# Performance work log

Hardware: AMD Instinct MI355X
Metric: run time of the kernel (lower is better)

## Reference

```python
import jax, jax.numpy as jnp
import numpy as np

N_QUBITS = 12
LAYERS = 3


def _apply(state, mats, axes):
    """Apply batched k-qubit gate. state: [B]+[2]*n complex64; mats: [B, 2^k, 2^k]; axes: state axes (1-based)."""
    k = len(axes)
    d = 2 ** k
    s = jnp.moveaxis(state, axes, tuple(range(1, k + 1)))
    shp = s.shape
    s = jnp.einsum('bij,bjk->bik', mats, s.reshape(shp[0], d, -1))
    return jnp.moveaxis(s.reshape(shp), tuple(range(1, k + 1)), axes)


def _ry(theta):
    # RY(theta) = [[cos(t/2), -sin(t/2)], [sin(t/2), cos(t/2)]], batched over B
    c = jnp.cos(theta / 2).astype(jnp.complex64)
    s = jnp.sin(theta / 2).astype(jnp.complex64)
    return jnp.stack([jnp.stack([c, -s], -1), jnp.stack([s, c], -1)], -2)


def _crx(theta):
    # CRX: identity on control=0 subspace, RX(theta) on control=1 subspace (basis order |ct>)
    c = jnp.cos(theta / 2).astype(jnp.complex64)
    s = (-1j) * jnp.sin(theta / 2).astype(jnp.complex64)
    o = jnp.ones_like(c)
    z = jnp.zeros_like(c)
    rows = [[o, z, z, z], [z, o, z, z], [z, z, c, s], [z, z, s, c]]
    return jnp.stack([jnp.stack(r, -1) for r in rows], -2)


def _circuit(state_re, state_im, params):
    B = params.shape[0]
    n = N_QUBITS
    state = (state_re + 1j * state_im).astype(jnp.complex64).reshape((B,) + (2,) * n)
    p = params.reshape(B, LAYERS, 4, n)  # param idx order: RY block, CRX block, RY block, CRX block
    for l in range(LAYERS):
        th = p[:, l]
        for w in range(n):
            state = _apply(state, _ry(th[:, 0, w]), (w + 1,))
        for i, w in enumerate(reversed(range(n))):
            state = _apply(state, _crx(th[:, 1, i]), (w + 1, ((w + 1) % n) + 1))
        for w in range(n):
            state = _apply(state, _ry(th[:, 2, w]), (w + 1,))
        for i, w in enumerate([n - 1] + list(range(n - 1))):
            state = _apply(state, _crx(th[:, 3, i]), (w + 1, ((w - 1) % n) + 1))
    state = state.reshape(B, -1)
    return jnp.stack([state.real, state.imag], -1)  # [B, 2^n, 2]


def setup_inputs() -> dict:
    key = jax.random.key(0)
    k1, k2, k3 = jax.random.split(key, 3)
    B = 128
    dim = 2 ** N_QUBITS
    return {
        'state_re': jax.random.normal(k1, (B, dim), jnp.float32),
        'state_im': jax.random.normal(k2, (B, dim), jnp.float32),
        'params': jax.random.normal(k3, (B, LAYERS * 4 * N_QUBITS), jnp.float32),
    }


def reference(state_re, state_im, params):
    return _circuit(state_re, state_im, params)
```

## Files before the change

### kernel.cpp

```cpp
#include <hip/hip_runtime.h>
#include <math.h>

#define DIM  4096
#define BLK  512
#define NPAR 144

typedef float v2f __attribute__((ext_vector_type(2)));

struct Ph { int reg[3]; int wav[3]; };
struct TMap { unsigned pk[9]; unsigned short so[8]; unsigned short rn[8]; };

constexpr int REGS[12][3] = {
  {11,0,1},{1,2,3},{3,4,5},{5,6,7},{7,8,9},{9,10,11},
  {11,0,1},{9,10,11},{7,8,9},{5,6,7},{3,4,5},{1,2,3}};

constexpr Ph phaseAt(int i) {
  Ph p = {};
  if (i == 0 || i == 37) {
    p.reg[0]=0; p.reg[1]=1; p.reg[2]=2;
    p.wav[0]=9; p.wav[1]=10; p.wav[2]=11;
    return p;
  }
  int e = (i - 1) % 12;
  for (int j = 0; j < 3; ++j) p.reg[j] = REGS[e][j];
  bool A = (e <= 2) || (e >= 10);
  p.wav[0] = A ? 6 : 2; p.wav[1] = A ? 7 : 3; p.wav[2] = A ? 8 : 4;
  return p;
}
constexpr bool inArr(const int* a, int n, int b) {
  for (int i = 0; i < n; ++i) if (a[i] == b) return true;
  return false;
}
constexpr int idxOf3(const int* a, int v) {
  for (int j = 0; j < 3; ++j) if (a[j] == v) return j;
  return -1;
}
constexpr bool isLoc(int t) {
  if (t == 0 || t == 36) return false;
  Ph a = phaseAt(t), b = phaseAt(t + 1);
  return a.wav[0]==b.wav[0] && a.wav[1]==b.wav[1] && a.wav[2]==b.wav[2];
}
constexpr int bufIdx(int t) {
  int k = 0;
  for (int u = 0; u <= t; ++u) if (!isLoc(u)) ++k;
  return (k + 1) & 1;
}
constexpr int sharedBit(Ph o, Ph n) {
  for (int j = 0; j < 3; ++j) if (inArr(n.reg, 3, o.reg[j])) return o.reg[j];
  return -1;
}

struct BuildOut { TMap m; int js, jn; bool ok; };

constexpr BuildOut buildT(Ph o, Ph n, bool local) {
  BuildOut R = {};
  R.ok = true;
  int s = sharedBit(o, n);
  if (s < 0) { R.ok = false; return R; }
  R.js = idxOf3(o.reg, s);
  R.jn = idxOf3(n.reg, s);
  if (R.js < 0 || R.jn < 0) { R.ok = false; return R; }
  bool lo[12] = {}, ln[12] = {};
  for (int b = 0; b < 12; ++b) {
    lo[b] = !inArr(o.reg,3,b) && !inArr(o.wav,3,b);
    ln[b] = !inArr(n.reg,3,b) && !inArr(n.wav,3,b);
  }
  int col[12] = {};
  bool uo[12] = {}, un[12] = {}, consumed[12] = {};
  col[s] = 1; consumed[s] = true;
  int row = 1;
  for (int b = 0; b < 12 && row < 4; ++b)
    if (lo[b] && ln[b] && !consumed[b]) { col[b] = 1 << row; uo[b]=un[b]=true; consumed[b]=true; ++row; }
  while (row < 4) {
    int a = -1, c = -1;
    for (int b = 0; b < 12; ++b) if (lo[b] && !uo[b] && !consumed[b]) { a = b; break; }
    for (int b = 0; b < 12; ++b) if (ln[b] && !un[b] && !consumed[b] && b != a) { c = b; break; }
    if (a < 0 || c < 0) { R.ok = false; return R; }
    col[a] |= 1 << row; col[c] |= 1 << row;
    uo[a]=true; un[c]=true; consumed[c]=true;
    ++row;
  }
  if (local) {
    for (int i = 0; i < 3; ++i) {
      if (consumed[o.wav[i]]) { R.ok = false; return R; }
      col[o.wav[i]] |= 1 << (9 + i);
      consumed[o.wav[i]] = true;
    }
    int rr = 4;
    for (int b = 0; b < 12; ++b) if (!consumed[b]) { col[b] |= 1 << rr; ++rr; }
    if (rr != 9) { R.ok = false; return R; }
  } else {
    int rr = 4;
    for (int b = 0; b < 12; ++b) if (!consumed[b]) { col[b] |= 1 << rr; ++rr; }
    if (rr != 12) { R.ok = false; return R; }
  }
  {
    int pv[12] = {}, pb[12] = {};
    int nr = 0;
    for (int b = 0; b < 12; ++b) {
      int v = col[b];
      for (int k = 0; k < nr; ++k) if (v & pb[k]) v ^= pv[k];
      if (v) { pb[nr] = v & (-v); pv[nr] = v; ++nr; }
    }
    if (nr != 12) { R.ok = false; return R; }
  }
  int Lo[6] = {}, Ln[6] = {};
  int i0 = 0, i1 = 0;
  for (int b = 0; b < 12; ++b) { if (lo[b]) Lo[i0++] = b; if (ln[b]) Ln[i1++] = b; }
  if (i0 != 6 || i1 != 6) { R.ok = false; return R; }
  for (int i = 0; i < 9; ++i) {
    unsigned po = (i < 6) ? (unsigned)col[Lo[i]] : (unsigned)col[o.wav[i-6]];
    unsigned pn = (i < 6) ? (unsigned)col[Ln[i]] : (unsigned)col[n.wav[i-6]];
    R.m.pk[i] = po | (pn << 16);
  }
  for (int r = 0; r < 8; ++r) {
    int a = 0, c = 0;
    for (int j = 0; j < 3; ++j)
      if ((r >> j) & 1) { a ^= col[o.reg[j]]; c ^= col[n.reg[j]]; }
    R.m.so[r] = (unsigned short)(a * 8);
    R.m.rn[r] = (unsigned short)(c * 8);
  }
  return R;
}

struct AllT { TMap t[37]; bool loc[37]; int buf[37]; int js[37]; int jn[37]; bool ok; };
constexpr AllT buildAll() {
  AllT A = {};
  A.ok = true;
  for (int t = 0; t < 37; ++t) {
    BuildOut b = buildT(phaseAt(t), phaseAt(t + 1), isLoc(t));
    A.t[t] = b.m;
    A.ok = A.ok && b.ok;
    A.loc[t] = isLoc(t);
    A.buf[t] = bufIdx(t);
    A.js[t] = b.js;
    A.jn[t] = b.jn;
  }
  return A;
}
constexpr AllT AT = buildAll();
static_assert(AT.ok, "slot-map construction failed");

__device__ __forceinline__ float rlf(float v, int l) {
  return __int_as_float(__builtin_amdgcn_readlane(__float_as_int(v), l));
}
template<int AO>
__device__ __forceinline__ v2f angAt(const float (&ct)[3], const float (&st)[3]) {
  v2f a;
  a.x = rlf(ct[AO >> 6], AO & 63);
  a.y = rlf(st[AO >> 6], AO & 63);
  return a;
}

template<int J>
__device__ __forceinline__ void ry8(v2f (&z)[8], v2f a) {
  const float c = a.x, s = a.y;
  #pragma unroll
  for (int p = 0; p < 4; ++p) {
    const int r0 = ((p & ~((1 << J) - 1)) << 1) | (p & ((1 << J) - 1));
    const int r1 = r0 | (1 << J);
    v2f u = z[r0], v = z[r1];
    z[r0] = c * u - s * v;
    z[r1] = s * u + c * v;
  }
}
template<int JC, int JT>
__device__ __forceinline__ void crx8(v2f (&z)[8], v2f a) {
  const float c = a.x, s = a.y;
  constexpr int MC = 1 << JC, MT = 1 << JT;
  constexpr int mlo = MC < MT ? MC : MT;
  constexpr int mhi = MC < MT ? MT : MC;
  #pragma unroll
  for (int p = 0; p < 2; ++p) {
    int q = ((p & ~(mlo - 1)) << 1) | (p & (mlo - 1));
    q = ((q & ~(mhi - 1)) << 1) | (q & (mhi - 1));
    const int r0 = q | MC, r1 = r0 | MT;
    v2f u = z[r0], v = z[r1];
    v2f n0, n1;
    n0.x = c * u.x + s * v.y;
    n0.y = c * u.y - s * v.x;
    n1.x = c * v.x + s * u.y;
    n1.y = c * v.y - s * u.x;
    z[r0] = n0; z[r1] = n1;
  }
}

template<int E, int L>
__device__ __forceinline__ void gates(v2f (&z)[8], const float (&ct)[3], const float (&st)[3]) {
#define A(k) (angAt<48 * L + (k)>(ct, st))
  if constexpr (E == 0)      { ry8<0>(z,A(0));  ry8<1>(z,A(11)); ry8<2>(z,A(10));
                               crx8<1,0>(z,A(12)); crx8<2,1>(z,A(13)); }
  else if constexpr (E == 1) { ry8<1>(z,A(9));  ry8<2>(z,A(8));
                               crx8<1,0>(z,A(14)); crx8<2,1>(z,A(15)); }
  else if constexpr (E == 2) { ry8<1>(z,A(7));  ry8<2>(z,A(6));
                               crx8<1,0>(z,A(16)); crx8<2,1>(z,A(17)); }
  else if constexpr (E == 3) { ry8<1>(z,A(5));  ry8<2>(z,A(4));
                               crx8<1,0>(z,A(18)); crx8<2,1>(z,A(19)); }
  else if constexpr (E == 4) { ry8<1>(z,A(3));  ry8<2>(z,A(2));
                               crx8<1,0>(z,A(20)); crx8<2,1>(z,A(21)); }
  else if constexpr (E == 5) { ry8<1>(z,A(1));
                               crx8<1,0>(z,A(22)); crx8<2,1>(z,A(23)); }
  else if constexpr (E == 6) { ry8<0>(z,A(24)); ry8<1>(z,A(35)); ry8<2>(z,A(34));
                               crx8<1,2>(z,A(36)); crx8<0,1>(z,A(37)); }
  else if constexpr (E == 7) { ry8<0>(z,A(26)); ry8<1>(z,A(25));
                               crx8<1,2>(z,A(38)); crx8<0,1>(z,A(39)); }
  else if constexpr (E == 8) { ry8<0>(z,A(28)); ry8<1>(z,A(27));
                               crx8<1,2>(z,A(40)); crx8<0,1>(z,A(41)); }
  else if constexpr (E == 9) { ry8<0>(z,A(30)); ry8<1>(z,A(29));
                               crx8<1,2>(z,A(42)); crx8<0,1>(z,A(43)); }
  else if constexpr (E == 10){ ry8<0>(z,A(32)); ry8<1>(z,A(31));
                               crx8<1,2>(z,A(44)); crx8<0,1>(z,A(45)); }
  else                       { ry8<1>(z,A(33));
                               crx8<1,2>(z,A(46)); crx8<0,1>(z,A(47)); }
#undef A
}

template<int T>
__device__ __forceinline__ void restage(v2f (&z)[8], int tid, char* Lb, char* C0, char* C1) {
  constexpr bool LOC = AT.loc[T];
  constexpr int JS = AT.js[T], JN = AT.jn[T];
  char* buf = LOC ? Lb : (AT.buf[T] ? C1 : C0);
  unsigned acc = 0;
  #pragma unroll
  for (int i = 0; i < 9; ++i)
    acc ^= (unsigned)(-((tid >> i) & 1)) & AT.t[T].pk[i];
  const unsigned bo = (acc & 0xfffu) << 3;
  const unsigned bn = ((acc >> 16) & 0xfffu) << 3;
  #pragma unroll
  for (int r = 0; r < 8; ++r) {
    if (r & (1 << JS)) continue;
    v2f z0 = z[r], z1 = z[r | (1 << JS)];
    float4 w; w.x = z0.x; w.y = z0.y; w.z = z1.x; w.w = z1.y;
    *(float4*)(buf + (bo ^ AT.t[T].so[r])) = w;
  }
  if (LOC) {
    asm volatile("" ::: "memory");
  } else {
    __syncthreads();
  }
  #pragma unroll
  for (int r = 0; r < 8; ++r) {
    if (r & (1 << JN)) continue;
    float4 w = *(const float4*)(buf + (bn ^ AT.t[T].rn[r]));
    v2f z0, z1;
    z0.x = w.x; z0.y = w.y;
    z1.x = w.z; z1.y = w.w;
    z[r] = z0;
    z[r | (1 << JN)] = z1;
  }
}

template<int L>
__device__ __forceinline__ void layer(v2f (&z)[8], int tid,
                                      const float (&ct)[3], const float (&st)[3],
                                      char* Lb, char* C0, char* C1) {
  gates<0, L>(z, ct, st);  restage<12*L + 1>(z, tid, Lb, C0, C1);
  gates<1, L>(z, ct, st);  restage<12*L + 2>(z, tid, Lb, C0, C1);
  gates<2, L>(z, ct, st);  restage<12*L + 3>(z, tid, Lb, C0, C1);
  gates<3, L>(z, ct, st);  restage<12*L + 4>(z, tid, Lb, C0, C1);
  gates<4, L>(z, ct, st);  restage<12*L + 5>(z, tid, Lb, C0, C1);
  gates<5, L>(z, ct, st);  restage<12*L + 6>(z, tid, Lb, C0, C1);
  gates<6, L>(z, ct, st);  restage<12*L + 7>(z, tid, Lb, C0, C1);
  gates<7, L>(z, ct, st);  restage<12*L + 8>(z, tid, Lb, C0, C1);
  gates<8, L>(z, ct, st);  restage<12*L + 9>(z, tid, Lb, C0, C1);
  gates<9, L>(z, ct, st);  restage<12*L + 10>(z, tid, Lb, C0, C1);
  gates<10, L>(z, ct, st); restage<12*L + 11>(z, tid, Lb, C0, C1);
  gates<11, L>(z, ct, st);
  if constexpr (L < 2) restage<12*L + 12>(z, tid, Lb, C0, C1);
}

__global__ __launch_bounds__(BLK) void ansatz_kernel(
    const float* __restrict__ sre, const float* __restrict__ sim,
    const float* __restrict__ params, float* __restrict__ out) {

  __shared__ alignas(16) v2f C0s[DIM], C1s[DIM], Ls[DIM];

  const int b = blockIdx.x, tid = threadIdx.x;
  char* C0 = (char*)C0s;
  char* C1 = (char*)C1s;
  char* Lb = (char*)Ls;

  float ct[3], st[3];
  {
    const int lane = tid & 63;
    #pragma unroll
    for (int j = 0; j < 3; ++j) {
      int idx = lane + 64 * j;
      int ci = (idx < NPAR) ? idx : 0;
      float th = params[(size_t)b * NPAR + ci];
      sincosf(0.5f * th, &st[j], &ct[j]);
    }
  }

  v2f z[8];
  {
    int base = ((tid & 15) << 2) | ((tid & 16) << 5) | ((tid & 32) << 5)
             | (tid & 64) | (tid & 128) | (tid & 256);
    const float4* pr = (const float4*)(sre + (size_t)b * DIM + base);
    const float4* pi = (const float4*)(sim + (size_t)b * DIM + base);
    float4 f0 = pr[0], f1 = pr[512];
    float4 g0 = pi[0], g1 = pi[512];
    z[0].x = f0.x; z[0].y = g0.x;  z[2].x = f0.y; z[2].y = g0.y;
    z[4].x = f0.z; z[4].y = g0.z;  z[6].x = f0.w; z[6].y = g0.w;
    z[1].x = f1.x; z[1].y = g1.x;  z[3].x = f1.y; z[3].y = g1.y;
    z[5].x = f1.z; z[5].y = g1.z;  z[7].x = f1.w; z[7].y = g1.w;
  }

  layer<0>(z, tid, ct, st, Lb, C0, C1);
  layer<1>(z, tid, ct, st, Lb, C0, C1);
  layer<2>(z, tid, ct, st, Lb, C0, C1);

  {
    int base = (tid & 1) | ((tid & 2) << 3) | ((tid & 4) << 3)
             | ((tid & 8) << 6) | ((tid & 16) << 6) | ((tid & 32) << 6)
             | (tid & 64) | (tid & 128) | (tid & 256);
    v2f* o2 = (v2f*)out + (size_t)b * DIM + base;
    #pragma unroll
    for (int r = 0; r < 8; ++r)
      o2[2 * r] = z[r];
  }
}

extern "C" void kernel_launch(void* const* d_in, const int* in_sizes, int n_in,
                              void* d_out, int out_size, void* d_ws, size_t ws_size,
                              hipStream_t stream) {
  const float* sre    = (const float*)d_in[0];
  const float* sim    = (const float*)d_in[1];
  const float* params = (const float*)d_in[2];
  float* out          = (float*)d_out;

  const int B = in_sizes[0] / DIM;
  ansatz_kernel<<<B, BLK, 0, stream>>>(sre, sim, params, out);
}
```

Baseline: 78.91 us.

## Pack two batch elements per 1024-thread block with single cross-wave buffer

Each block now handles two batch elements with 1024 threads, launching B/2 blocks. The ping-pong pair of cross-wave LDS buffers is replaced by a single buffer guarded by an extra barrier before each write. The aim is to fill more CUs' wave slots per block and cut LDS per element. The cost is that barriers now span both elements, so the two halves stall on each other, and there is one more __syncthreads per non-local restage. With B=128 this yields only 64 blocks, so fewer CUs may be occupied.

```diff
diff --git a/kernel.cpp b/kernel.cpp
--- a/kernel.cpp
+++ b/kernel.cpp
@@ -2,7 +2,7 @@
 #include <math.h>
 
 #define DIM  4096
-#define BLK  512
+#define BLK  1024
 #define NPAR 144
 
 typedef float v2f __attribute__((ext_vector_type(2)));
@@ -39,11 +39,6 @@
   if (t == 0 || t == 36) return false;
   Ph a = phaseAt(t), b = phaseAt(t + 1);
   return a.wav[0]==b.wav[0] && a.wav[1]==b.wav[1] && a.wav[2]==b.wav[2];
-}
-constexpr int bufIdx(int t) {
-  int k = 0;
-  for (int u = 0; u <= t; ++u) if (!isLoc(u)) ++k;
-  return (k + 1) & 1;
 }
 constexpr int sharedBit(Ph o, Ph n) {
   for (int j = 0; j < 3; ++j) if (inArr(n.reg, 3, o.reg[j])) return o.reg[j];
@@ -123,7 +118,7 @@
   return R;
 }
 
-struct AllT { TMap t[37]; bool loc[37]; int buf[37]; int js[37]; int jn[37]; bool ok; };
+struct AllT { TMap t[37]; bool loc[37]; int js[37]; int jn[37]; bool ok; };
 constexpr AllT buildAll() {
   AllT A = {};
   A.ok = true;
@@ -132,7 +127,6 @@
     A.t[t] = b.m;
     A.ok = A.ok && b.ok;
     A.loc[t] = isLoc(t);
-    A.buf[t] = bufIdx(t);
     A.js[t] = b.js;
     A.jn[t] = b.jn;
   }
@@ -216,16 +210,17 @@
 }
 
 template<int T>
-__device__ __forceinline__ void restage(v2f (&z)[8], int tid, char* Lb, char* C0, char* C1) {
+__device__ __forceinline__ void restage(v2f (&z)[8], int t9, char* Lb, char* C) {
   constexpr bool LOC = AT.loc[T];
   constexpr int JS = AT.js[T], JN = AT.jn[T];
-  char* buf = LOC ? Lb : (AT.buf[T] ? C1 : C0);
+  char* buf = LOC ? Lb : C;
   unsigned acc = 0;
   #pragma unroll
   for (int i = 0; i < 9; ++i)
-    acc ^= (unsigned)(-((tid >> i) & 1)) & AT.t[T].pk[i];
+    acc ^= (unsigned)(-((t9 >> i) & 1)) & AT.t[T].pk[i];
   const unsigned bo = (acc & 0xfffu) << 3;
   const unsigned bn = ((acc >> 16) & 0xfffu) << 3;
+  if constexpr (!LOC) __syncthreads();
   #pragma unroll
   for (int r = 0; r < 8; ++r) {
     if (r & (1 << JS)) continue;
@@ -233,7 +228,7 @@
     float4 w; w.x = z0.x; w.y = z0.y; w.z = z1.x; w.w = z1.y;
     *(float4*)(buf + (bo ^ AT.t[T].so[r])) = w;
   }
-  if (LOC) {
+  if constexpr (LOC) {
     asm volatile("" ::: "memory");
   } else {
     __syncthreads();
@@ -251,34 +246,37 @@
 }
 
 template<int L>
-__device__ __forceinline__ void layer(v2f (&z)[8], int tid,
+__device__ __forceinline__ void layer(v2f (&z)[8], int t9,
                                       const float (&ct)[3], const float (&st)[3],
-                                      char* Lb, char* C0, char* C1) {
-  gates<0, L>(z, ct, st);  restage<12*L + 1>(z, tid, Lb, C0, C1);
-  gates<1, L>(z, ct, st);  restage<12*L + 2>(z, tid, Lb, C0, C1);
-  gates<2, L>(z, ct, st);  restage<12*L + 3>(z, tid, Lb, C0, C1);
-  gates<3, L>(z, ct, st);  restage<12*L + 4>(z, tid, Lb, C0, C1);
-  gates<4, L>(z, ct, st);  restage<12*L + 5>(z, tid, Lb, C0, C1);
-  gates<5, L>(z, ct, st);  restage<12*L + 6>(z, tid, Lb, C0, C1);
-  gates<6, L>(z, ct, st);  restage<12*L + 7>(z, tid, Lb, C0, C1);
-  gates<7, L>(z, ct, st);  restage<12*L + 8>(z, tid, Lb, C0, C1);
-  gates<8, L>(z, ct, st);  restage<12*L + 9>(z, tid, Lb, C0, C1);
-  gates<9, L>(z, ct, st);  restage<12*L + 10>(z, tid, Lb, C0, C1);
-  gates<10, L>(z, ct, st); restage<12*L + 11>(z, tid, Lb, C0, C1);
+                                      char* Lb, char* C) {
+  gates<0, L>(z, ct, st);  restage<12*L + 1>(z, t9, Lb, C);
+  gates<1, L>(z, ct, st);  restage<12*L + 2>(z, t9, Lb, C);
+  gates<2, L>(z, ct, st);  restage<12*L + 3>(z, t9, Lb, C);
+  gates<3, L>(z, ct, st);  restage<12*L + 4>(z, t9, Lb, C);
+  gates<4, L>(z, ct, st);  restage<12*L + 5>(z, t9, Lb, C);
+  gates<5, L>(z, ct, st);  restage<12*L + 6>(z, t9, Lb, C);
+  gates<6, L>(z, ct, st);  restage<12*L + 7>(z, t9, Lb, C);
+  gates<7, L>(z, ct, st);  restage<12*L + 8>(z, t9, Lb, C);
+  gates<8, L>(z, ct, st);  restage<12*L + 9>(z, t9, Lb, C);
+  gates<9, L>(z, ct, st);  restage<12*L + 10>(z, t9, Lb, C);
+  gates<10, L>(z, ct, st); restage<12*L + 11>(z, t9, Lb, C);
   gates<11, L>(z, ct, st);
-  if constexpr (L < 2) restage<12*L + 12>(z, tid, Lb, C0, C1);
-}
-
-__global__ __launch_bounds__(BLK) void ansatz_kernel(
+  if constexpr (L < 2) restage<12*L + 12>(z, t9, Lb, C);
+}
+
+__global__ __launch_bounds__(BLK, 4) void ansatz_kernel(
     const float* __restrict__ sre, const float* __restrict__ sim,
     const float* __restrict__ params, float* __restrict__ out) {
 
-  __shared__ alignas(16) v2f C0s[DIM], C1s[DIM], Ls[DIM];
-
-  const int b = blockIdx.x, tid = threadIdx.x;
-  char* C0 = (char*)C0s;
-  char* C1 = (char*)C1s;
-  char* Lb = (char*)Ls;
+  __shared__ alignas(16) v2f Lb2[2][DIM];
+  __shared__ alignas(16) v2f Cb2[2][DIM];
+
+  const int tid = threadIdx.x;
+  const int el  = tid >> 9;
+  const int t9  = tid & 511;
+  const int b2  = (blockIdx.x << 1) | el;
+  char* Lb = (char*)Lb2[el];
+  char* C  = (char*)Cb2[el];
 
   float ct[3], st[3];
   {
@@ -287,17 +285,17 @@
     for (int j = 0; j < 3; ++j) {
       int idx = lane + 64 * j;
       int ci = (idx < NPAR) ? idx : 0;
-      float th = params[(size_t)b * NPAR + ci];
+      float th = params[(size_t)b2 * NPAR + ci];
       sincosf(0.5f * th, &st[j], &ct[j]);
     }
   }
 
   v2f z[8];
   {
-    int base = ((tid & 15) << 2) | ((tid & 16) << 5) | ((tid & 32) << 5)
-             | (tid & 64) | (tid & 128) | (tid & 256);
-    const float4* pr = (const float4*)(sre + (size_t)b * DIM + base);
-    const float4* pi = (const float4*)(sim + (size_t)b * DIM + base);
+    int base = ((t9 & 15) << 2) | ((t9 & 16) << 5) | ((t9 & 32) << 5)
+             | (t9 & 64) | (t9 & 128) | (t9 & 256);
+    const float4* pr = (const float4*)(sre + (size_t)b2 * DIM + base);
+    const float4* pi = (const float4*)(sim + (size_t)b2 * DIM + base);
     float4 f0 = pr[0], f1 = pr[512];
     float4 g0 = pi[0], g1 = pi[512];
     z[0].x = f0.x; z[0].y = g0.x;  z[2].x = f0.y; z[2].y = g0.y;
@@ -306,15 +304,15 @@
     z[5].x = f1.z; z[5].y = g1.z;  z[7].x = f1.w; z[7].y = g1.w;
   }
 
-  layer<0>(z, tid, ct, st, Lb, C0, C1);
-  layer<1>(z, tid, ct, st, Lb, C0, C1);
-  layer<2>(z, tid, ct, st, Lb, C0, C1);
+  layer<0>(z, t9, ct, st, Lb, C);
+  layer<1>(z, t9, ct, st, Lb, C);
+  layer<2>(z, t9, ct, st, Lb, C);
 
   {
-    int base = (tid & 1) | ((tid & 2) << 3) | ((tid & 4) << 3)
-             | ((tid & 8) << 6) | ((tid & 16) << 6) | ((tid & 32) << 6)
-             | (tid & 64) | (tid & 128) | (tid & 256);
-    v2f* o2 = (v2f*)out + (size_t)b * DIM + base;
+    int base = (t9 & 1) | ((t9 & 2) << 3) | ((t9 & 4) << 3)
+             | ((t9 & 8) << 6) | ((t9 & 16) << 6) | ((t9 & 32) << 6)
+             | (t9 & 64) | (t9 & 128) | (t9 & 256);
+    v2f* o2 = (v2f*)out + (size_t)b2 * DIM + base;
     #pragma unroll
     for (int r = 0; r < 8; ++r)
       o2[2 * r] = z[r];
@@ -330,5 +328,5 @@
   float* out          = (float*)d_out;
 
   const int B = in_sizes[0] / DIM;
-  ansatz_kernel<<<B, BLK, 0, stream>>>(sre, sim, params, out);
-}
+  ansatz_kernel<<<B / 2, BLK, 0, stream>>>(sre, sim, params, out);
+}
```

Result: slower. 92.40 us (+17.1%).
